# Optimization experiments

Measured on AMD Instinct MI355X. Metric: run time of the kernel, lower is better.

The kernel has to match this reference:

```python
import jax, jax.numpy as jnp
import numpy as np

KH = KW = 3
STRIDE = 1
PAD = 1
DIL = 1


def _bilinear_sample(x, py, px):
    """Zero-padded bilinear sampling.
    x: [B, C, H, W]; py, px: [B, K2, Ho, Wo] float sample coords.
    returns [B, C, K2, Ho, Wo].
    """
    B, C, H, W = x.shape
    y0 = jnp.floor(py)
    x0 = jnp.floor(px)
    wy1 = py - y0
    wx1 = px - x0
    wy0 = 1.0 - wy1
    wx0 = 1.0 - wx1
    xf = x.reshape(B, C, H * W)

    def gather(iy, ix):
        valid = (iy >= 0) & (iy <= H - 1) & (ix >= 0) & (ix <= W - 1)
        iyc = jnp.clip(iy, 0, H - 1).astype(jnp.int32)
        ixc = jnp.clip(ix, 0, W - 1).astype(jnp.int32)
        idx = (iyc * W + ixc).reshape(B, 1, -1)  # [B,1,K2*Ho*Wo]
        v = jnp.take_along_axis(xf, idx, axis=2)
        v = v.reshape(B, C, *iy.shape[1:])
        return v * valid[:, None].astype(x.dtype)

    return (gather(y0, x0) * (wy0 * wx0)[:, None]
            + gather(y0, x0 + 1) * (wy0 * wx1)[:, None]
            + gather(y0 + 1, x0) * (wy1 * wx0)[:, None]
            + gather(y0 + 1, x0 + 1) * (wy1 * wx1)[:, None])


def setup_inputs() -> dict:
    key = jax.random.key(0)
    k1, k2, k3, k4 = jax.random.split(key, 4)
    B, C, H, W = 8, 64, 128, 128
    Cout = 64
    K2 = KH * KW
    x = jax.random.normal(k1, (B, C, H, W), dtype=jnp.float32)
    offset = jax.random.normal(k2, (B, 2 * K2, H, W), dtype=jnp.float32)
    mask = jax.random.uniform(k3, (B, K2, H, W), dtype=jnp.float32)
    n = C * KH * KW
    stdv = 1.0 / np.sqrt(n)
    weight = jax.random.uniform(k4, (Cout, C, KH, KW), dtype=jnp.float32,
                                minval=-stdv, maxval=stdv)
    bias = jnp.zeros((Cout,), dtype=jnp.float32)
    return {"x": x, "offset": offset, "mask": mask, "weight": weight, "bias": bias}


def reference(x, offset, mask, weight, bias):
    B, C, H, W = x.shape
    Cout, Cin, kh, kw = weight.shape
    K2 = kh * kw
    Ho = (H + 2 * PAD - (DIL * (kh - 1) + 1)) // STRIDE + 1
    Wo = (W + 2 * PAD - (DIL * (kw - 1) + 1)) // STRIDE + 1
    # offset channels come interleaved per kernel location: ::2 -> x, 1::2 -> y
    off = offset.reshape(B, K2, 2, Ho, Wo)
    dx = off[:, :, 0]  # [B,K2,Ho,Wo]
    dy = off[:, :, 1]
    base_y = (STRIDE * jnp.arange(Ho) - PAD).astype(x.dtype)  # [Ho]
    base_x = (STRIDE * jnp.arange(Wo) - PAD).astype(x.dtype)  # [Wo]
    ky = (DIL * jnp.arange(kh)).astype(x.dtype)
    kx = (DIL * jnp.arange(kw)).astype(x.dtype)
    koff_y = jnp.repeat(ky, kw)  # [K2]
    koff_x = jnp.tile(kx, kh)    # [K2]
    py = base_y[None, None, :, None] + koff_y[None, :, None, None] + dy
    px = base_x[None, None, None, :] + koff_x[None, :, None, None] + dx
    sampled = _bilinear_sample(x, py, px)          # [B,C,K2,Ho,Wo]
    sampled = sampled * mask[:, None]              # modulation
    w = weight.reshape(Cout, Cin * K2)
    cols = sampled.reshape(B, Cin * K2, Ho, Wo)
    out = jnp.einsum('bqhw,oq->bohw', cols, w) + bias[None, :, None, None]
    return out
```

## Files before the change

kernel.cpp:

```cpp
#include <hip/hip_runtime.h>
#include <hip/hip_bf16.h>
#include <hip/hip_fp16.h>


constexpr int B    = 8;
constexpr int C    = 64;
constexpr int H    = 128;
constexpr int W    = 128;
constexpr int COUT = 64;
constexpr int K2   = 9;
constexpr int HW   = H * W;
constexpr int TPX  = 32;

typedef __attribute__((ext_vector_type(8))) short    short8;
typedef __attribute__((ext_vector_type(8))) _Float16 f16x8;
typedef __attribute__((ext_vector_type(4))) float    f32x4;

constexpr int LDSS = 72;

#define LDS_BARRIER() asm volatile("s_waitcnt lgkmcnt(0)\n\ts_barrier" ::: "memory")

__global__ __launch_bounds__(256) void transpose_x_kernel(
    const float* __restrict__ x, short* __restrict__ xt) {
    __shared__ float tbuf[64][65];
    const int blk  = blockIdx.x;
    const int b    = blk >> 8;
    const int hwb  = (blk & 255) * 64;
    const int lane = threadIdx.x & 63;
    const int grp  = threadIdx.x >> 6;
    const float* xb = x + (size_t)b * C * HW;
#pragma unroll
    for (int r = 0; r < 16; ++r) {
        const int c = grp * 16 + r;
        tbuf[c][lane] = xb[c * HW + hwb + lane];
    }
    __syncthreads();
    short* xo = xt + (size_t)b * HW * C;
#pragma unroll
    for (int r = 0; r < 16; ++r) {
        const int hw_l = grp * 16 + r;
        union { __half h; short s; } u;
        u.h = __float2half(tbuf[lane][hw_l]);
        xo[(size_t)(hwb + hw_l) * C + lane] = u.s;
    }
}

__global__ __launch_bounds__(256) void pack_w_kernel(
    const float* __restrict__ w, short* __restrict__ wfrag) {
    int id = blockIdx.x * blockDim.x + threadIdx.x;
    if (id >= COUT * C * K2) return;
    const int j    = id & 7;
    const int lane = (id >> 3) & 63;
    const int mt   = (id >> 9) & 3;
    const int kk   = (id >> 11) & 1;
    const int k    = id >> 12;
    const int m    = mt * 16 + (lane & 15);
    const int q    = lane >> 4;
    const int c    = kk * 32 + q * 8 + j;
    union { __half h; short s; } u;
    u.h = __float2half(w[(m * C + c) * K2 + k]);
    wfrag[id] = u.s;
}

__global__ __launch_bounds__(256, 8) void mdcn_pc_kernel(
    const short* __restrict__ xt,
    const float* __restrict__ offset,
    const float* __restrict__ mask,
    const short* __restrict__ wfrag,
    const float* __restrict__ bias,
    float* __restrict__ out) {

    __shared__ short   smem[2][TPX * LDSS];
    __shared__ ushort4 pidx[K2 * TPX];
    __shared__ uint2   pwts[K2 * TPX];

    const int wg   = blockIdx.x;
    const int b    = wg & 7;
    const int t    = wg >> 3;
    const int ho   = t >> 2;
    const int px0  = (t & 3) * TPX;

    const int tid  = threadIdx.x;
    const int wave = tid >> 6;

    for (int f = tid; f < K2 * TPX; f += 256) {
        const int k = f >> 5;
        const int i = f & 31;
        const int wo = px0 + i;
        const int ky = k / 3, kx = k % 3;
        const float dx = offset[(((size_t)b * 2 * K2 + 2 * k    ) * H + ho) * W + wo];
        const float dy = offset[(((size_t)b * 2 * K2 + 2 * k + 1) * H + ho) * W + wo];
        const float mm = mask  [(((size_t)b * K2     + k        ) * H + ho) * W + wo];
        const float py = (float)(ho - 1 + ky) + dy;
        const float px = (float)(wo - 1 + kx) + dx;
        const float y0f = floorf(py), x0f = floorf(px);
        const float wy1 = py - y0f,   wx1 = px - x0f;
        const float wy0 = 1.0f - wy1, wx0 = 1.0f - wx1;
        const int iy0 = (int)y0f, ix0 = (int)x0f;
        const int iy1 = iy0 + 1,  ix1 = ix0 + 1;
        const bool vy0 = (iy0 >= 0) & (iy0 < H);
        const bool vy1 = (iy1 >= 0) & (iy1 < H);
        const bool vx0 = (ix0 >= 0) & (ix0 < W);
        const bool vx1 = (ix1 >= 0) & (ix1 < W);
        const float w00 = (vy0 & vx0) ? wy0 * wx0 * mm : 0.0f;
        const float w01 = (vy0 & vx1) ? wy0 * wx1 * mm : 0.0f;
        const float w10 = (vy1 & vx0) ? wy1 * wx0 * mm : 0.0f;
        const float w11 = (vy1 & vx1) ? wy1 * wx1 * mm : 0.0f;
        union { __half2 h2; unsigned u; } p01, p23;
        p01.h2 = __floats2half2_rn(w00, w01);
        p23.h2 = __floats2half2_rn(w10, w11);
        const int cy0 = min(max(iy0, 0), H - 1);
        const int cy1 = min(max(iy1, 0), H - 1);
        const int cx0 = min(max(ix0, 0), W - 1);
        const int cx1 = min(max(ix1, 0), W - 1);
        ushort4 bv;
        bv.x = (unsigned short)(cy0 * W + cx0);
        bv.y = (unsigned short)(cy0 * W + cx1);
        bv.z = (unsigned short)(cy1 * W + cx0);
        bv.w = (unsigned short)(cy1 * W + cx1);
        pidx[f] = bv;
        pwts[f] = uint2{p01.u, p23.u};
    }
    __syncthreads();

    if (wave < 2) {
        const int spx = tid >> 2;
        const int cq  = (tid & 3) * 16;
        const char* xb =
            (const char*)(xt + (size_t)b * HW * C) + cq * 2;

        for (int k = 0; k < K2; ++k) {
            const ushort4 bi = pidx[k * TPX + spx];
            const uint2   wu = pwts[k * TPX + spx];
            union HU { unsigned u; __half2 h2; };
            HU t01{wu.x}, t23{wu.y};
            const __half2 w0 = __half2half2(__low2half (t01.h2));
            const __half2 w1 = __half2half2(__high2half(t01.h2));
            const __half2 w2 = __half2half2(__low2half (t23.h2));
            const __half2 w3 = __half2half2(__high2half(t23.h2));
            const short* s00 = (const short*)(xb + ((int)bi.x << 7));
            const short* s01 = (const short*)(xb + ((int)bi.y << 7));
            const short* s10 = (const short*)(xb + ((int)bi.z << 7));
            const short* s11 = (const short*)(xb + ((int)bi.w << 7));

            short* dst = &smem[k & 1][spx * LDSS + cq];
#pragma unroll
            for (int h = 0; h < 2; ++h) {
                union U8 { short8 s; __half2 h2[4]; };
                const U8 g00{*(const short8*)(s00 + h * 8)};
                const U8 g01{*(const short8*)(s01 + h * 8)};
                const U8 g10{*(const short8*)(s10 + h * 8)};
                const U8 g11{*(const short8*)(s11 + h * 8)};
                U8 rr;
#pragma unroll
                for (int p = 0; p < 4; ++p) {
                    rr.h2[p] = __hfma2(g11.h2[p], w3,
                               __hfma2(g10.h2[p], w2,
                               __hfma2(g01.h2[p], w1,
                               __hmul2(g00.h2[p], w0))));
                }
                *(short8*)(dst + h * 8) = rr.s;
            }
            LDS_BARRIER();
        }
    } else {
        const int w    = wave - 2;
        const int lane = tid & 63;
        const int col  = lane & 15;
        const int q    = lane >> 4;
        const f16x8* wf = (const f16x8*)wfrag;

        f32x4 acc[2][2];
#pragma unroll
        for (int m = 0; m < 2; ++m)
#pragma unroll
            for (int n = 0; n < 2; ++n) acc[m][n] = (f32x4)0.0f;

        f16x8 afa[4], afb[4];
#pragma unroll
        for (int m = 0; m < 2; ++m)
#pragma unroll
            for (int kk = 0; kk < 2; ++kk)
                afa[m * 2 + kk] = wf[(kk * 4 + 2 * w + m) * 64 + lane];

#pragma unroll
        for (int k = 0; k < K2; ++k) {
            auto& af  = (k & 1) ? afb : afa;
            auto& afn = (k & 1) ? afa : afb;
            LDS_BARRIER();
            if (k + 1 < K2) {
#pragma unroll
                for (int m = 0; m < 2; ++m)
#pragma unroll
                    for (int kk = 0; kk < 2; ++kk)
                        afn[m * 2 + kk] =
                            wf[((k + 1) * 8 + kk * 4 + 2 * w + m) * 64 + lane];
            }
#pragma unroll
            for (int kk = 0; kk < 2; ++kk) {
#pragma unroll
                for (int n = 0; n < 2; ++n) {
                    const f16x8 bfrag = *(const f16x8*)(
                        &smem[k & 1][(n * 16 + col) * LDSS + kk * 32 + q * 8]);
#pragma unroll
                    for (int m = 0; m < 2; ++m)
                        acc[m][n] = __builtin_amdgcn_mfma_f32_16x16x32_f16(
                            af[m * 2 + kk], bfrag, acc[m][n], 0, 0, 0);
                }
            }
        }

#pragma unroll
        for (int m = 0; m < 2; ++m) {
#pragma unroll
            for (int n = 0; n < 2; ++n) {
                const int wo = px0 + n * 16 + col;
#pragma unroll
                for (int r = 0; r < 4; ++r) {
                    const int o = (2 * w + m) * 16 + q * 4 + r;
                    out[(((size_t)b * COUT + o) * H + ho) * W + wo] =
                        acc[m][n][r] + bias[o];
                }
            }
        }
    }
}

__global__ __launch_bounds__(256) void mdcn_direct_kernel(
    const float* __restrict__ x, const float* __restrict__ offset,
    const float* __restrict__ mask, const float* __restrict__ wsrc,
    const float* __restrict__ bias, float* __restrict__ out) {
    const int p  = blockIdx.x * blockDim.x + threadIdx.x;
    const int wo = p & (W - 1);
    const int ho = (p >> 7) & (H - 1);
    const int b  = p >> 14;
    float acc[COUT];
#pragma unroll
    for (int o = 0; o < COUT; ++o) acc[o] = bias[o];
    const float* xb = x + b * C * HW;
    for (int k = 0; k < K2; ++k) {
        const int ky = k / 3, kx = k % 3;
        const float dx = offset[((b * 2 * K2 + 2 * k    ) * H + ho) * W + wo];
        const float dy = offset[((b * 2 * K2 + 2 * k + 1) * H + ho) * W + wo];
        const float m  = mask  [((b * K2     + k        ) * H + ho) * W + wo];
        const float py = (float)(ho - 1 + ky) + dy;
        const float px = (float)(wo - 1 + kx) + dx;
        const float y0f = floorf(py), x0f = floorf(px);
        const float wy1 = py - y0f, wx1 = px - x0f;
        const float wy0 = 1.0f - wy1, wx0 = 1.0f - wx1;
        const int iy0 = (int)y0f, ix0 = (int)x0f;
        const int iy1 = iy0 + 1, ix1 = ix0 + 1;
        const bool vy0 = (iy0 >= 0) & (iy0 < H);
        const bool vy1 = (iy1 >= 0) & (iy1 < H);
        const bool vx0 = (ix0 >= 0) & (ix0 < W);
        const bool vx1 = (ix1 >= 0) & (ix1 < W);
        const float w00 = (vy0 & vx0) ? wy0 * wx0 * m : 0.0f;
        const float w01 = (vy0 & vx1) ? wy0 * wx1 * m : 0.0f;
        const float w10 = (vy1 & vx0) ? wy1 * wx0 * m : 0.0f;
        const float w11 = (vy1 & vx1) ? wy1 * wx1 * m : 0.0f;
        const int cy0 = min(max(iy0, 0), H - 1);
        const int cy1 = min(max(iy1, 0), H - 1);
        const int cx0 = min(max(ix0, 0), W - 1);
        const int cx1 = min(max(ix1, 0), W - 1);
        const int o00 = cy0 * W + cx0, o01 = cy0 * W + cx1;
        const int o10 = cy1 * W + cx0, o11 = cy1 * W + cx1;
        for (int c = 0; c < C; ++c) {
            const float* xp = xb + c * HW;
            const float val = w00 * xp[o00] + w01 * xp[o01] +
                              w10 * xp[o10] + w11 * xp[o11];
#pragma unroll
            for (int o = 0; o < COUT; ++o)
                acc[o] += wsrc[(o * C + c) * K2 + k] * val;
        }
    }
    float* op = out + ((size_t)b * COUT) * HW + ho * W + wo;
#pragma unroll
    for (int o = 0; o < COUT; ++o) op[o * HW] = acc[o];
}

extern "C" void kernel_launch(void* const* d_in, const int* in_sizes, int n_in,
                              void* d_out, int out_size, void* d_ws, size_t ws_size,
                              hipStream_t stream) {
    const float* x      = (const float*)d_in[0];
    const float* offset = (const float*)d_in[1];
    const float* mask   = (const float*)d_in[2];
    const float* weight = (const float*)d_in[3];
    const float* bias   = (const float*)d_in[4];
    float* out          = (float*)d_out;

    const size_t xt_bytes = (size_t)B * HW * C * sizeof(short);
    const size_t wf_bytes = (size_t)COUT * C * K2 * sizeof(short);
    if (ws_size >= xt_bytes + wf_bytes) {
        short* xt    = (short*)d_ws;
        short* wfrag = (short*)((char*)d_ws + xt_bytes);
        transpose_x_kernel<<<B * (HW / 64), 256, 0, stream>>>(x, xt);
        pack_w_kernel<<<(COUT * C * K2 + 255) / 256, 256, 0, stream>>>(weight, wfrag);
        mdcn_pc_kernel<<<4 * B * H, 256, 0, stream>>>(xt, offset, mask, wfrag, bias, out);
    } else {
        mdcn_direct_kernel<<<(B * HW) / 256, 256, 0, stream>>>(
            x, offset, mask, weight, bias, out);
    }
}
```

Measured before the change: 136.8 us.

## Batch three kernel taps per barrier in producer-consumer deformable conv

```diff
diff --git a/kernel.cpp b/kernel.cpp
--- a/kernel.cpp
+++ b/kernel.cpp
@@ -62,7 +62,7 @@
     wfrag[id] = u.s;
 }
 
-__global__ __launch_bounds__(256, 8) void mdcn_pc_kernel(
+__global__ __launch_bounds__(256, 4) void mdcn_pc_kernel(
     const short* __restrict__ xt,
     const float* __restrict__ offset,
     const float* __restrict__ mask,
@@ -70,7 +70,7 @@
     const float* __restrict__ bias,
     float* __restrict__ out) {
 
-    __shared__ short   smem[2][TPX * LDSS];
+    __shared__ short   smem[6][TPX * LDSS];
     __shared__ ushort4 pidx[K2 * TPX];
     __shared__ uint2   pwts[K2 * TPX];
 
@@ -129,37 +129,62 @@
         const char* xb =
             (const char*)(xt + (size_t)b * HW * C) + cq * 2;
 
-        for (int k = 0; k < K2; ++k) {
-            const ushort4 bi = pidx[k * TPX + spx];
-            const uint2   wu = pwts[k * TPX + spx];
-            union HU { unsigned u; __half2 h2; };
-            HU t01{wu.x}, t23{wu.y};
-            const __half2 w0 = __half2half2(__low2half (t01.h2));
-            const __half2 w1 = __half2half2(__high2half(t01.h2));
-            const __half2 w2 = __half2half2(__low2half (t23.h2));
-            const __half2 w3 = __half2half2(__high2half(t23.h2));
-            const short* s00 = (const short*)(xb + ((int)bi.x << 7));
-            const short* s01 = (const short*)(xb + ((int)bi.y << 7));
-            const short* s10 = (const short*)(xb + ((int)bi.z << 7));
-            const short* s11 = (const short*)(xb + ((int)bi.w << 7));
-
-            short* dst = &smem[k & 1][spx * LDSS + cq];
-#pragma unroll
-            for (int h = 0; h < 2; ++h) {
-                union U8 { short8 s; __half2 h2[4]; };
-                const U8 g00{*(const short8*)(s00 + h * 8)};
-                const U8 g01{*(const short8*)(s01 + h * 8)};
-                const U8 g10{*(const short8*)(s10 + h * 8)};
-                const U8 g11{*(const short8*)(s11 + h * 8)};
-                U8 rr;
-#pragma unroll
-                for (int p = 0; p < 4; ++p) {
-                    rr.h2[p] = __hfma2(g11.h2[p], w3,
-                               __hfma2(g10.h2[p], w2,
-                               __hfma2(g01.h2[p], w1,
-                               __hmul2(g00.h2[p], w0))));
+#pragma unroll
+        for (int batch = 0; batch < 3; ++batch) {
+            const int base  = batch * 3;
+            const int sbase = (batch & 1) * 3;
+
+            ushort4 bi[3];
+            uint2   wu[3];
+#pragma unroll
+            for (int tt = 0; tt < 3; ++tt) {
+                bi[tt] = pidx[(base + tt) * TPX + spx];
+                wu[tt] = pwts[(base + tt) * TPX + spx];
+            }
+
+            short8 g[3][8];
+#pragma unroll
+            for (int tt = 0; tt < 3; ++tt) {
+                const short* s00 = (const short*)(xb + ((int)bi[tt].x << 7));
+                const short* s01 = (const short*)(xb + ((int)bi[tt].y << 7));
+                const short* s10 = (const short*)(xb + ((int)bi[tt].z << 7));
+                const short* s11 = (const short*)(xb + ((int)bi[tt].w << 7));
+                g[tt][0] = *(const short8*)(s00);
+                g[tt][1] = *(const short8*)(s01);
+                g[tt][2] = *(const short8*)(s10);
+                g[tt][3] = *(const short8*)(s11);
+                g[tt][4] = *(const short8*)(s00 + 8);
+                g[tt][5] = *(const short8*)(s01 + 8);
+                g[tt][6] = *(const short8*)(s10 + 8);
+                g[tt][7] = *(const short8*)(s11 + 8);
+            }
+
+#pragma unroll
+            for (int tt = 0; tt < 3; ++tt) {
+                union HU { unsigned u; __half2 h2; };
+                HU t01{wu[tt].x}, t23{wu[tt].y};
+                const __half2 w0 = __half2half2(__low2half (t01.h2));
+                const __half2 w1 = __half2half2(__high2half(t01.h2));
+                const __half2 w2 = __half2half2(__low2half (t23.h2));
+                const __half2 w3 = __half2half2(__high2half(t23.h2));
+                short* dst = &smem[sbase + tt][spx * LDSS + cq];
+#pragma unroll
+                for (int h = 0; h < 2; ++h) {
+                    union U8 { short8 s; __half2 h2[4]; };
+                    const U8 g00{g[tt][h * 4 + 0]};
+                    const U8 g01{g[tt][h * 4 + 1]};
+                    const U8 g10{g[tt][h * 4 + 2]};
+                    const U8 g11{g[tt][h * 4 + 3]};
+                    U8 rr;
+#pragma unroll
+                    for (int p = 0; p < 4; ++p) {
+                        rr.h2[p] = __hfma2(g11.h2[p], w3,
+                                   __hfma2(g10.h2[p], w2,
+                                   __hfma2(g01.h2[p], w1,
+                                   __hmul2(g00.h2[p], w0))));
+                    }
+                    *(short8*)(dst + h * 8) = rr.s;
                 }
-                *(short8*)(dst + h * 8) = rr.s;
             }
             LDS_BARRIER();
         }
@@ -176,36 +201,36 @@
 #pragma unroll
             for (int n = 0; n < 2; ++n) acc[m][n] = (f32x4)0.0f;
 
-        f16x8 afa[4], afb[4];
-#pragma unroll
-        for (int m = 0; m < 2; ++m)
-#pragma unroll
-            for (int kk = 0; kk < 2; ++kk)
-                afa[m * 2 + kk] = wf[(kk * 4 + 2 * w + m) * 64 + lane];
-
-#pragma unroll
-        for (int k = 0; k < K2; ++k) {
-            auto& af  = (k & 1) ? afb : afa;
-            auto& afn = (k & 1) ? afa : afb;
+#pragma unroll
+        for (int batch = 0; batch < 3; ++batch) {
+            const int base  = batch * 3;
+            const int sbase = (batch & 1) * 3;
+
+            f16x8 af[3][4];
+#pragma unroll
+            for (int tt = 0; tt < 3; ++tt)
+#pragma unroll
+                for (int m = 0; m < 2; ++m)
+#pragma unroll
+                    for (int kk = 0; kk < 2; ++kk)
+                        af[tt][m * 2 + kk] =
+                            wf[((base + tt) * 8 + kk * 4 + 2 * w + m) * 64 + lane];
+
             LDS_BARRIER();
-            if (k + 1 < K2) {
-#pragma unroll
-                for (int m = 0; m < 2; ++m)
-#pragma unroll
-                    for (int kk = 0; kk < 2; ++kk)
-                        afn[m * 2 + kk] =
-                            wf[((k + 1) * 8 + kk * 4 + 2 * w + m) * 64 + lane];
-            }
-#pragma unroll
-            for (int kk = 0; kk < 2; ++kk) {
-#pragma unroll
-                for (int n = 0; n < 2; ++n) {
-                    const f16x8 bfrag = *(const f16x8*)(
-                        &smem[k & 1][(n * 16 + col) * LDSS + kk * 32 + q * 8]);
-#pragma unroll
-                    for (int m = 0; m < 2; ++m)
-                        acc[m][n] = __builtin_amdgcn_mfma_f32_16x16x32_f16(
-                            af[m * 2 + kk], bfrag, acc[m][n], 0, 0, 0);
+
+#pragma unroll
+            for (int tt = 0; tt < 3; ++tt) {
+#pragma unroll
+                for (int kk = 0; kk < 2; ++kk) {
+#pragma unroll
+                    for (int n = 0; n < 2; ++n) {
+                        const f16x8 bfrag = *(const f16x8*)(
+                            &smem[sbase + tt][(n * 16 + col) * LDSS + kk * 32 + q * 8]);
+#pragma unroll
+                        for (int m = 0; m < 2; ++m)
+                            acc[m][n] = __builtin_amdgcn_mfma_f32_16x16x32_f16(
+                                af[tt][m * 2 + kk], bfrag, acc[m][n], 0, 0, 0);
+                    }
                 }
             }
         }
```

New measurement: 135.2 us. No clear change (-1.1%).

## Stage input neighborhood tile in LDS for bilinear gathers with global fallback

Applied to the files above, without the earlier changes.

```diff
diff --git a/kernel.cpp b/kernel.cpp
--- a/kernel.cpp
+++ b/kernel.cpp
@@ -11,6 +11,12 @@
 constexpr int K2   = 9;
 constexpr int HW   = H * W;
 constexpr int TPX  = 32;
+
+constexpr int SROWS = 9;
+constexpr int SCOLS = 44;
+constexpr int SCELL = 72;
+constexpr int NCELL = SROWS * SCOLS;
+constexpr int NCHNK = NCELL * 8;
 
 typedef __attribute__((ext_vector_type(8))) short    short8;
 typedef __attribute__((ext_vector_type(8))) _Float16 f16x8;
@@ -62,7 +68,7 @@
     wfrag[id] = u.s;
 }
 
-__global__ __launch_bounds__(256, 8) void mdcn_pc_kernel(
+__global__ __launch_bounds__(256, 4) void mdcn_pc_kernel(
     const short* __restrict__ xt,
     const float* __restrict__ offset,
     const float* __restrict__ mask,
@@ -70,6 +76,7 @@
     const float* __restrict__ bias,
     float* __restrict__ out) {
 
+    __shared__ short   stage[NCELL * SCELL];
     __shared__ short   smem[2][TPX * LDSS];
     __shared__ ushort4 pidx[K2 * TPX];
     __shared__ uint2   pwts[K2 * TPX];
@@ -82,6 +89,21 @@
 
     const int tid  = threadIdx.x;
     const int wave = tid >> 6;
+
+    const int row0 = ho - 4;
+    const int col0 = px0 - 7;
+    const short* xball = xt + (size_t)b * HW * C;
+
+    for (int n = tid; n < NCHNK; n += 256) {
+        const int cell = n >> 3;
+        const int chs  = n & 7;
+        const int r    = cell / SCOLS;
+        const int c    = cell % SCOLS;
+        const int sr   = min(max(row0 + r, 0), H - 1);
+        const int sc   = min(max(col0 + c, 0), W - 1);
+        *(short8*)&stage[cell * SCELL + chs * 8] =
+            *(const short8*)(xball + ((sr << 7) + sc) * 64 + chs * 8);
+    }
 
     for (int f = tid; f < K2 * TPX; f += 256) {
         const int k = f >> 5;
@@ -125,9 +147,8 @@
 
     if (wave < 2) {
         const int spx = tid >> 2;
-        const int cq  = (tid & 3) * 16;
-        const char* xb =
-            (const char*)(xt + (size_t)b * HW * C) + cq * 2;
+        const int cq  = tid & 3;
+        const int cqs = cq * 16;
 
         for (int k = 0; k < K2; ++k) {
             const ushort4 bi = pidx[k * TPX + spx];
@@ -138,19 +159,34 @@
             const __half2 w1 = __half2half2(__high2half(t01.h2));
             const __half2 w2 = __half2half2(__low2half (t23.h2));
             const __half2 w3 = __half2half2(__high2half(t23.h2));
-            const short* s00 = (const short*)(xb + ((int)bi.x << 7));
-            const short* s01 = (const short*)(xb + ((int)bi.y << 7));
-            const short* s10 = (const short*)(xb + ((int)bi.z << 7));
-            const short* s11 = (const short*)(xb + ((int)bi.w << 7));
-
-            short* dst = &smem[k & 1][spx * LDSS + cq];
+
+            short8 g[8];
+#pragma unroll
+            for (int j = 0; j < 4; ++j) {
+                const int idx = (j == 0) ? (int)bi.x : (j == 1) ? (int)bi.y
+                              : (j == 2) ? (int)bi.z : (int)bi.w;
+                const int cy = idx >> 7, cx = idx & 127;
+                const unsigned r = (unsigned)(cy - row0);
+                const unsigned c = (unsigned)(cx - col0);
+                if (r < (unsigned)SROWS && c < (unsigned)SCOLS) {
+                    const short* s = &stage[(r * SCOLS + c) * SCELL + cqs];
+                    g[j * 2]     = *(const short8*)(s);
+                    g[j * 2 + 1] = *(const short8*)(s + 8);
+                } else {
+                    const short* s = xball + idx * 64 + cqs;
+                    g[j * 2]     = *(const short8*)(s);
+                    g[j * 2 + 1] = *(const short8*)(s + 8);
+                }
+            }
+
+            short* dst = &smem[k & 1][spx * LDSS + cqs];
 #pragma unroll
             for (int h = 0; h < 2; ++h) {
                 union U8 { short8 s; __half2 h2[4]; };
-                const U8 g00{*(const short8*)(s00 + h * 8)};
-                const U8 g01{*(const short8*)(s01 + h * 8)};
-                const U8 g10{*(const short8*)(s10 + h * 8)};
-                const U8 g11{*(const short8*)(s11 + h * 8)};
+                const U8 g00{g[0 + h]};
+                const U8 g01{g[2 + h]};
+                const U8 g10{g[4 + h]};
+                const U8 g11{g[6 + h]};
                 U8 rr;
 #pragma unroll
                 for (int p = 0; p < 4; ++p) {
```

New measurement: 172.8 us. 1.26x slower.
